# Kernel optimization log

Hardware: AMD Instinct MI355X
Metric: run time of the kernel (lower is better)

The kernel has to match this reference:

```python
import jax, jax.numpy as jnp
import numpy as np

B, T, D = 2, 1024, 1024   # batch, seq, d_model
E, F = 8, 4096            # n_experts, expert hidden (4*d_model)


def setup_inputs() -> dict:
    key = jax.random.key(0)
    k1, k2, k3, k4, k5 = jax.random.split(key, 5)
    x = jax.random.normal(k1, (B, T, D), dtype=jnp.float32)
    token_mask = jax.random.randint(k2, (B, T), 0, 2).astype(jnp.int32)
    router_w = jax.random.normal(k3, (E, D), dtype=jnp.float32) * (1.0 / np.sqrt(D))
    w1 = jax.random.normal(k4, (E, D, F), dtype=jnp.float32) * (1.0 / np.sqrt(D))
    w2 = jax.random.normal(k5, (E, F, D), dtype=jnp.float32) * (1.0 / np.sqrt(F))
    return {"x": x, "token_mask": token_mask, "router_w": router_w, "w1": w1, "w2": w2}


def reference(x, token_mask, router_w, w1, w2):
    b, t, d = x.shape
    n_exp = router_w.shape[0]
    xf = x.reshape(b * t, d)                       # [N, D]
    # top-1 router
    logits = xf @ router_w.T                       # [N, E]
    probs = jax.nn.softmax(logits, axis=-1)
    expert_idx = jnp.argmax(probs, axis=-1)        # [N]
    gate = jnp.take_along_axis(probs, expert_idx[:, None], axis=1)[:, 0]  # [N]
    # expert FFNs: each token routed to exactly one expert (dense masked combine)
    y = jnp.zeros_like(xf)
    for e in range(n_exp):
        he = jnp.maximum(xf @ w1[e], 0.0) @ w2[e]  # [N, D]
        y = jnp.where(expert_idx[:, None] == e, he, y)
    # gate scaling + token masking (masked rows stay exactly zero,
    # matching torch's zero-init y_flat_all + index_copy_)
    mask = token_mask.reshape(b * t).astype(x.dtype)
    out = y * (gate * mask)[:, None]
    return out.reshape(b, t, d)
```

## Files before the change

### kernel.cpp

```cpp
#include <hip/hip_runtime.h>
#include <hip/hip_bf16.h>

#define NTOK 2048
#define DM 1024
#define NEXP 8
#define FFN 4096
#define BM 64
#define BN 64
#define BK 64
#define ASTR 72
#define MT1 8
#define G2_SPLIT 4

typedef __bf16 bf16x8 __attribute__((ext_vector_type(8)));
typedef __bf16 bf16x4 __attribute__((ext_vector_type(4)));
typedef float f32x4 __attribute__((ext_vector_type(4)));

__device__ __forceinline__ bf16x8 zero8() {
  bf16x8 z;
#pragma unroll
  for (int j = 0; j < 8; j++) z[j] = (__bf16)0.f;
  return z;
}

__device__ __forceinline__ bf16x8 readB(const char* BsB, int row, int kh, int quad) {
  return *(const bf16x8*)(BsB + row * 144 +
                          ((((kh << 2) + quad) ^ (row >> 3)) << 4));
}

#define STOREB4() do {                                                   \
    const float* p0 = (const float*)&br0;                                \
    const float* p1 = (const float*)&br1;                                \
    const float* p2 = (const float*)&br2;                                \
    const float* p3 = (const float*)&br3;                                \
    _Pragma("unroll") for (int c = 0; c < 4; ++c) {                      \
      bf16x4 o;                                                          \
      o[0] = (__bf16)p0[c]; o[1] = (__bf16)p1[c];                        \
      o[2] = (__bf16)p2[c]; o[3] = (__bf16)p3[c];                        \
      *(bf16x4*)(bb + c * 144) = o;                                      \
    } } while (0)

__global__ __launch_bounds__(256) void router_gather(
    const float* __restrict__ x, const int* __restrict__ mask,
    const float* __restrict__ rw, int* __restrict__ counts,
    int* __restrict__ tlist, float* __restrict__ gateE,
    __bf16* __restrict__ xg)
{
  int wid = threadIdx.x >> 6, lane = threadIdx.x & 63;
  int t = blockIdx.x * 4 + wid;

  const float* xr = x + (size_t)t * DM;
  float xv[16];
#pragma unroll
  for (int i = 0; i < 4; i++) {
    const float4 v = *(const float4*)(xr + lane * 16 + i * 4);
    xv[i * 4 + 0] = v.x; xv[i * 4 + 1] = v.y;
    xv[i * 4 + 2] = v.z; xv[i * 4 + 3] = v.w;
  }

  float acc[NEXP];
#pragma unroll
  for (int e = 0; e < NEXP; e++) {
    float a = 0.f;
    const float* rwe = rw + e * DM + lane * 16;
#pragma unroll
    for (int i = 0; i < 4; i++) {
      const float4 r = *(const float4*)(rwe + i * 4);
      a += xv[i*4+0]*r.x + xv[i*4+1]*r.y + xv[i*4+2]*r.z + xv[i*4+3]*r.w;
    }
    acc[e] = a;
  }
#pragma unroll
  for (int e = 0; e < NEXP; e++)
#pragma unroll
    for (int s = 1; s < 64; s <<= 1) acc[e] += __shfl_xor(acc[e], s, 64);

  int pack = -1;
  if (lane == 0 && mask[t] != 0) {
    float m = acc[0]; int am = 0;
#pragma unroll
    for (int e = 1; e < NEXP; e++) if (acc[e] > m) { m = acc[e]; am = e; }
    float s = 0.f;
#pragma unroll
    for (int e = 0; e < NEXP; e++) s += __expf(acc[e] - m);
    int slot = atomicAdd(&counts[am], 1);
    tlist[am * NTOK + slot] = t;
    gateE[am * NTOK + slot] = 1.0f / s;
    pack = am * NTOK + slot;
  }
  pack = __shfl(pack, 0, 64);
  if (pack >= 0) {
    __bf16* dst = xg + (size_t)pack * DM + lane * 16;
    bf16x8 o0, o1;
#pragma unroll
    for (int j = 0; j < 8; j++) {
      o0[j] = (__bf16)xv[j];
      o1[j] = (__bf16)xv[8 + j];
    }
    *(bf16x8*)dst = o0;
    *(bf16x8*)(dst + 8) = o1;
  }
}

__global__ __launch_bounds__(256) void moe_gemm1(
    const __bf16* __restrict__ xg, const float* __restrict__ w1,
    const int* __restrict__ counts, const int* __restrict__ tlist,
    __bf16* __restrict__ h)
{
  int bx = blockIdx.x;
  int nt = bx & 63, mt = (bx >> 6) & (MT1 - 1), e = bx >> 9;
  int cnt = counts[e];
  if (mt * BM >= cnt) return;
  int n0 = nt * BN;

  __shared__ __bf16 As[BM][ASTR];
  __shared__ char   Bs[64 * 144];
  __shared__ int    toks[BM];

  int tid = threadIdx.x, lane = tid & 63, w = tid >> 6;
  int wm = w >> 1, wn = w & 1;
  int r16 = lane & 15, quad = lane >> 4;
  int rsw = r16 >> 1;
  char* bb = Bs + (r16 << 2) * 144 +
             (((((w << 1) + (quad >> 1))) ^ rsw) << 4) + ((quad & 1) << 3);

  const __bf16* xge = xg + (size_t)e * NTOK * DM;
  const float*  w1e = w1 + (size_t)e * DM * FFN;

  int ar = tid >> 2;
  int ak = (tid & 3) << 4;
  const float* bptr = w1e + (size_t)(w * 16 + quad * 4) * FFN + n0 + (r16 << 2);

  bf16x8 a0r, a1r;
  float4 br0, br1, br2, br3;

#define LOADG1(kb) do {                                                   \
    a0r = av ? *(const bf16x8*)(aptr + (kb))     : zero8();               \
    a1r = av ? *(const bf16x8*)(aptr + (kb) + 8) : zero8();               \
    br0 = *(const float4*)(bptr + (size_t)((kb) + 0) * FFN);              \
    br1 = *(const float4*)(bptr + (size_t)((kb) + 1) * FFN);              \
    br2 = *(const float4*)(bptr + (size_t)((kb) + 2) * FFN);              \
    br3 = *(const float4*)(bptr + (size_t)((kb) + 3) * FFN);              \
  } while (0)

  for (int m0 = mt * BM; m0 < cnt; m0 += MT1 * BM) {
    bool av = (m0 + ar) < cnt;
    const __bf16* aptr = xge + (size_t)(m0 + ar) * DM + ak;

    f32x4 acc[2][2] = {};
    LOADG1(0);
    const int T = DM / BK;
    for (int t = 0; t < T; t++) {
      *(bf16x8*)&As[ar][ak]     = a0r;
      *(bf16x8*)&As[ar][ak + 8] = a1r;
      STOREB4();
      __syncthreads();
      if (t + 1 < T) LOADG1((t + 1) * BK);
#pragma unroll
      for (int kh = 0; kh < 2; kh++) {
        int ks = kh * 32 + (quad << 3);
        bf16x8 aA = *(const bf16x8*)&As[wm * 32 + r16][ks];
        bf16x8 aB = *(const bf16x8*)&As[wm * 32 + 16 + r16][ks];
        bf16x8 bA = readB(Bs, wn * 32 + r16, kh, quad);
        bf16x8 bB = readB(Bs, wn * 32 + 16 + r16, kh, quad);
        acc[0][0] = __builtin_amdgcn_mfma_f32_16x16x32_bf16(aA, bA, acc[0][0], 0, 0, 0);
        acc[0][1] = __builtin_amdgcn_mfma_f32_16x16x32_bf16(aA, bB, acc[0][1], 0, 0, 0);
        acc[1][0] = __builtin_amdgcn_mfma_f32_16x16x32_bf16(aB, bA, acc[1][0], 0, 0, 0);
        acc[1][1] = __builtin_amdgcn_mfma_f32_16x16x32_bf16(aB, bB, acc[1][1], 0, 0, 0);
      }
      __syncthreads();
    }

    if (tid < BM) toks[tid] = (m0 + tid < cnt) ? tlist[e * NTOK + m0 + tid] : -1;
    __syncthreads();

#pragma unroll
    for (int mf = 0; mf < 2; mf++) {
#pragma unroll
      for (int i = 0; i < 4; i++) {
        int row = wm * 32 + mf * 16 + (quad << 2) + i;
        int tok = toks[row];
        if (tok >= 0) {
          __bf16* hp = h + (size_t)tok * FFN + n0 + wn * 32 + r16;
          hp[0]  = (__bf16)fmaxf(acc[mf][0][i], 0.f);
          hp[16] = (__bf16)fmaxf(acc[mf][1][i], 0.f);
        }
      }
    }
    __syncthreads();
  }
#undef LOADG1
}

__global__ __launch_bounds__(256) void moe_gemm2(
    const __bf16* __restrict__ h, const float* __restrict__ w2,
    const int* __restrict__ counts, const int* __restrict__ tlist,
    const float* __restrict__ gateE, float* __restrict__ out)
{
  int bx = blockIdx.x;
  int nt = bx & 15, mt = (bx >> 4) & (MT1 - 1), e = (bx >> 7) & 7, sp = bx >> 10;
  int cnt = counts[e];
  if (mt * BM >= cnt) return;
  int n0 = nt * BN;
  int ksp = sp * (FFN / G2_SPLIT);

  __shared__ __bf16 As[BM][ASTR];
  __shared__ char   Bs[64 * 144];
  __shared__ int    toks[BM];
  __shared__ float  gts[BM];

  int tid = threadIdx.x, lane = tid & 63, w = tid >> 6;
  int wm = w >> 1, wn = w & 1;
  int r16 = lane & 15, quad = lane >> 4;
  int rsw = r16 >> 1;
  char* bb = Bs + (r16 << 2) * 144 +
             (((((w << 1) + (quad >> 1))) ^ rsw) << 4) + ((quad & 1) << 3);

  const float* w2e = w2 + (size_t)e * FFN * DM;
  int ar = tid >> 2;
  int ak = (tid & 3) << 4;
  const float* bptr = w2e + (size_t)(ksp + w * 16 + quad * 4) * DM + n0 + (r16 << 2);

  bf16x8 a0r, a1r;
  float4 br0, br1, br2, br3;

#define LOADG2(kb) do {                                                   \
    a0r = av ? *(const bf16x8*)(aptr + (kb))     : zero8();               \
    a1r = av ? *(const bf16x8*)(aptr + (kb) + 8) : zero8();               \
    br0 = *(const float4*)(bptr + (size_t)((kb) + 0) * DM);               \
    br1 = *(const float4*)(bptr + (size_t)((kb) + 1) * DM);               \
    br2 = *(const float4*)(bptr + (size_t)((kb) + 2) * DM);               \
    br3 = *(const float4*)(bptr + (size_t)((kb) + 3) * DM);               \
  } while (0)

  for (int m0 = mt * BM; m0 < cnt; m0 += MT1 * BM) {
    if (tid < BM) {
      bool v = (m0 + tid) < cnt;
      toks[tid] = v ? tlist[e * NTOK + m0 + tid] : -1;
      gts[tid]  = v ? gateE[e * NTOK + m0 + tid] : 0.f;
    }
    __syncthreads();

    int tok0 = toks[ar];
    bool av = tok0 >= 0;
    const __bf16* aptr = h + (size_t)(av ? tok0 : 0) * FFN + ksp + ak;

    f32x4 acc[2][2] = {};
    LOADG2(0);
    const int T = (FFN / G2_SPLIT) / BK;
    for (int t = 0; t < T; t++) {
      *(bf16x8*)&As[ar][ak]     = a0r;
      *(bf16x8*)&As[ar][ak + 8] = a1r;
      STOREB4();
      __syncthreads();
      if (t + 1 < T) LOADG2((t + 1) * BK);
#pragma unroll
      for (int kh = 0; kh < 2; kh++) {
        int ks = kh * 32 + (quad << 3);
        bf16x8 aA = *(const bf16x8*)&As[wm * 32 + r16][ks];
        bf16x8 aB = *(const bf16x8*)&As[wm * 32 + 16 + r16][ks];
        bf16x8 bA = readB(Bs, wn * 32 + r16, kh, quad);
        bf16x8 bB = readB(Bs, wn * 32 + 16 + r16, kh, quad);
        acc[0][0] = __builtin_amdgcn_mfma_f32_16x16x32_bf16(aA, bA, acc[0][0], 0, 0, 0);
        acc[0][1] = __builtin_amdgcn_mfma_f32_16x16x32_bf16(aA, bB, acc[0][1], 0, 0, 0);
        acc[1][0] = __builtin_amdgcn_mfma_f32_16x16x32_bf16(aB, bA, acc[1][0], 0, 0, 0);
        acc[1][1] = __builtin_amdgcn_mfma_f32_16x16x32_bf16(aB, bB, acc[1][1], 0, 0, 0);
      }
      __syncthreads();
    }

#pragma unroll
    for (int mf = 0; mf < 2; mf++) {
#pragma unroll
      for (int i = 0; i < 4; i++) {
        int row = wm * 32 + mf * 16 + (quad << 2) + i;
        int tok = toks[row];
        if (tok >= 0) {
          float g = gts[row];
          float* op = out + (size_t)tok * DM + n0 + wn * 32 + r16;
          __hip_atomic_fetch_add(op, acc[mf][0][i] * g,
                                 __ATOMIC_RELAXED, __HIP_MEMORY_SCOPE_AGENT);
          __hip_atomic_fetch_add(op + 16, acc[mf][1][i] * g,
                                 __ATOMIC_RELAXED, __HIP_MEMORY_SCOPE_AGENT);
        }
      }
    }
    __syncthreads();
  }
#undef LOADG2
}

extern "C" void kernel_launch(void* const* d_in, const int* in_sizes, int n_in,
                              void* d_out, int out_size, void* d_ws, size_t ws_size,
                              hipStream_t stream) {
  const float* x    = (const float*)d_in[0];
  const int*   mask = (const int*)d_in[1];
  const float* rw   = (const float*)d_in[2];
  const float* w1   = (const float*)d_in[3];
  const float* w2   = (const float*)d_in[4];
  float* out = (float*)d_out;

  char* ws = (char*)d_ws;
  int*    counts = (int*)ws;
  int*    tlist  = (int*)(ws + 1024);
  float*  gateE  = (float*)(ws + 1024 + 65536);
  __bf16* xg     = (__bf16*)(ws + 132096);
  __bf16* h      = (__bf16*)(ws + 132096 +
                             (size_t)NEXP * NTOK * DM * 2);

  hipMemsetAsync(counts, 0, 1024, stream);
  hipMemsetAsync(out, 0, (size_t)out_size * sizeof(float), stream);

  router_gather<<<NTOK / 4, 256, 0, stream>>>(x, mask, rw, counts, tlist, gateE, xg);
  moe_gemm1<<<NEXP * MT1 * (FFN / BN), 256, 0, stream>>>(xg, w1, counts, tlist, h);
  moe_gemm2<<<G2_SPLIT * NEXP * MT1 * (DM / BN), 256, 0, stream>>>(
      h, w2, counts, tlist, gateE, out);
}
```

Before: 124.6 us.

## Double-buffer LDS tiles and shrink M-tile grid with interleaved block mapping

Both expert GEMMs now keep two LDS buffers for the A and B tiles and prefetch two K-steps ahead, so each iteration needs one barrier instead of two and global loads overlap the MFMA work. The grid drops from 8 M-tile slots per expert/N-tile to 2, each block looping over more token tiles. Block indices are remapped so the two M-slots of neighbouring N-tiles interleave. Launch bounds also request 4 blocks per CU. This cuts blocks that exit immediately but adds LDS use and register pressure, and gives each block more serial work.

```diff
diff --git a/kernel.cpp b/kernel.cpp
--- a/kernel.cpp
+++ b/kernel.cpp
@@ -9,8 +9,8 @@
 #define BN 64
 #define BK 64
 #define ASTR 72
-#define MT1 8
 #define G2_SPLIT 4
+#define BBYTES 9216
 
 typedef __bf16 bf16x8 __attribute__((ext_vector_type(8)));
 typedef __bf16 bf16x4 __attribute__((ext_vector_type(4)));
@@ -28,7 +28,7 @@
                           ((((kh << 2) + quad) ^ (row >> 3)) << 4));
 }
 
-#define STOREB4() do {                                                   \
+#define STOREB4(bbp) do {                                                \
     const float* p0 = (const float*)&br0;                                \
     const float* p1 = (const float*)&br1;                                \
     const float* p2 = (const float*)&br2;                                \
@@ -37,7 +37,7 @@
       bf16x4 o;                                                          \
       o[0] = (__bf16)p0[c]; o[1] = (__bf16)p1[c];                        \
       o[2] = (__bf16)p2[c]; o[3] = (__bf16)p3[c];                        \
-      *(bf16x4*)(bb + c * 144) = o;                                      \
+      *(bf16x4*)((bbp) + c * 144) = o;                                   \
     } } while (0)
 
 __global__ __launch_bounds__(256) void router_gather(
@@ -102,27 +102,29 @@
   }
 }
 
-__global__ __launch_bounds__(256) void moe_gemm1(
+__global__ __launch_bounds__(256, 4) void moe_gemm1(
     const __bf16* __restrict__ xg, const float* __restrict__ w1,
     const int* __restrict__ counts, const int* __restrict__ tlist,
     __bf16* __restrict__ h)
 {
   int bx = blockIdx.x;
-  int nt = bx & 63, mt = (bx >> 6) & (MT1 - 1), e = bx >> 9;
+  int low3 = bx & 7, mt = (bx >> 3) & 1;
+  int idx = ((bx >> 4) << 3) | low3;
+  int e = idx >> 6, nt = idx & 63;
   int cnt = counts[e];
   if (mt * BM >= cnt) return;
   int n0 = nt * BN;
 
-  __shared__ __bf16 As[BM][ASTR];
-  __shared__ char   Bs[64 * 144];
+  __shared__ __bf16 As[2][BM][ASTR];
+  __shared__ char   Bs[2][BBYTES];
   __shared__ int    toks[BM];
 
   int tid = threadIdx.x, lane = tid & 63, w = tid >> 6;
   int wm = w >> 1, wn = w & 1;
   int r16 = lane & 15, quad = lane >> 4;
   int rsw = r16 >> 1;
-  char* bb = Bs + (r16 << 2) * 144 +
-             (((((w << 1) + (quad >> 1))) ^ rsw) << 4) + ((quad & 1) << 3);
+  char* bb0 = Bs[0] + (r16 << 2) * 144 +
+              (((((w << 1) + (quad >> 1))) ^ rsw) << 4) + ((quad & 1) << 3);
 
   const __bf16* xge = xg + (size_t)e * NTOK * DM;
   const float*  w1e = w1 + (size_t)e * DM * FFN;
@@ -143,31 +145,40 @@
     br3 = *(const float4*)(bptr + (size_t)((kb) + 3) * FFN);              \
   } while (0)
 
-  for (int m0 = mt * BM; m0 < cnt; m0 += MT1 * BM) {
+#define WRITEAB1(PAR) do {                                                \
+    *(bf16x8*)&As[PAR][ar][ak]     = a0r;                                 \
+    *(bf16x8*)&As[PAR][ar][ak + 8] = a1r;                                 \
+    STOREB4(bb0 + (PAR) * BBYTES);                                        \
+  } while (0)
+
+#define MFMA8(PAR) do {                                                   \
+    _Pragma("unroll") for (int kh = 0; kh < 2; kh++) {                    \
+      int ks = kh * 32 + (quad << 3);                                     \
+      bf16x8 aA = *(const bf16x8*)&As[PAR][wm * 32 + r16][ks];            \
+      bf16x8 aB = *(const bf16x8*)&As[PAR][wm * 32 + 16 + r16][ks];       \
+      bf16x8 bA = readB(Bs[PAR], wn * 32 + r16, kh, quad);                \
+      bf16x8 bB = readB(Bs[PAR], wn * 32 + 16 + r16, kh, quad);           \
+      acc[0][0] = __builtin_amdgcn_mfma_f32_16x16x32_bf16(aA, bA, acc[0][0], 0, 0, 0); \
+      acc[0][1] = __builtin_amdgcn_mfma_f32_16x16x32_bf16(aA, bB, acc[0][1], 0, 0, 0); \
+      acc[1][0] = __builtin_amdgcn_mfma_f32_16x16x32_bf16(aB, bA, acc[1][0], 0, 0, 0); \
+      acc[1][1] = __builtin_amdgcn_mfma_f32_16x16x32_bf16(aB, bB, acc[1][1], 0, 0, 0); \
+    } } while (0)
+
+  for (int m0 = mt * BM; m0 < cnt; m0 += 2 * BM) {
     bool av = (m0 + ar) < cnt;
     const __bf16* aptr = xge + (size_t)(m0 + ar) * DM + ak;
 
     f32x4 acc[2][2] = {};
     LOADG1(0);
+    WRITEAB1(0);
+    LOADG1(BK);
+    __syncthreads();
     const int T = DM / BK;
     for (int t = 0; t < T; t++) {
-      *(bf16x8*)&As[ar][ak]     = a0r;
-      *(bf16x8*)&As[ar][ak + 8] = a1r;
-      STOREB4();
-      __syncthreads();
-      if (t + 1 < T) LOADG1((t + 1) * BK);
-#pragma unroll
-      for (int kh = 0; kh < 2; kh++) {
-        int ks = kh * 32 + (quad << 3);
-        bf16x8 aA = *(const bf16x8*)&As[wm * 32 + r16][ks];
-        bf16x8 aB = *(const bf16x8*)&As[wm * 32 + 16 + r16][ks];
-        bf16x8 bA = readB(Bs, wn * 32 + r16, kh, quad);
-        bf16x8 bB = readB(Bs, wn * 32 + 16 + r16, kh, quad);
-        acc[0][0] = __builtin_amdgcn_mfma_f32_16x16x32_bf16(aA, bA, acc[0][0], 0, 0, 0);
-        acc[0][1] = __builtin_amdgcn_mfma_f32_16x16x32_bf16(aA, bB, acc[0][1], 0, 0, 0);
-        acc[1][0] = __builtin_amdgcn_mfma_f32_16x16x32_bf16(aB, bA, acc[1][0], 0, 0, 0);
-        acc[1][1] = __builtin_amdgcn_mfma_f32_16x16x32_bf16(aB, bB, acc[1][1], 0, 0, 0);
-      }
+      const int par = t & 1;
+      if (t + 1 < T) WRITEAB1(par ^ 1);
+      if (t + 2 < T) LOADG1((t + 2) * BK);
+      MFMA8(par);
       __syncthreads();
     }
 
@@ -189,23 +200,27 @@
     }
     __syncthreads();
   }
+#undef MFMA8
+#undef WRITEAB1
 #undef LOADG1
 }
 
-__global__ __launch_bounds__(256) void moe_gemm2(
+__global__ __launch_bounds__(256, 4) void moe_gemm2(
     const __bf16* __restrict__ h, const float* __restrict__ w2,
     const int* __restrict__ counts, const int* __restrict__ tlist,
     const float* __restrict__ gateE, float* __restrict__ out)
 {
   int bx = blockIdx.x;
-  int nt = bx & 15, mt = (bx >> 4) & (MT1 - 1), e = (bx >> 7) & 7, sp = bx >> 10;
+  int low3 = bx & 7, mt = (bx >> 3) & 1;
+  int idx = ((bx >> 4) << 3) | low3;
+  int nt = idx & 15, e = (idx >> 4) & 7, sp = idx >> 7;
   int cnt = counts[e];
   if (mt * BM >= cnt) return;
   int n0 = nt * BN;
   int ksp = sp * (FFN / G2_SPLIT);
 
-  __shared__ __bf16 As[BM][ASTR];
-  __shared__ char   Bs[64 * 144];
+  __shared__ __bf16 As[2][BM][ASTR];
+  __shared__ char   Bs[2][BBYTES];
   __shared__ int    toks[BM];
   __shared__ float  gts[BM];
 
@@ -213,8 +228,8 @@
   int wm = w >> 1, wn = w & 1;
   int r16 = lane & 15, quad = lane >> 4;
   int rsw = r16 >> 1;
-  char* bb = Bs + (r16 << 2) * 144 +
-             (((((w << 1) + (quad >> 1))) ^ rsw) << 4) + ((quad & 1) << 3);
+  char* bb0 = Bs[0] + (r16 << 2) * 144 +
+              (((((w << 1) + (quad >> 1))) ^ rsw) << 4) + ((quad & 1) << 3);
 
   const float* w2e = w2 + (size_t)e * FFN * DM;
   int ar = tid >> 2;
@@ -233,7 +248,26 @@
     br3 = *(const float4*)(bptr + (size_t)((kb) + 3) * DM);               \
   } while (0)
 
-  for (int m0 = mt * BM; m0 < cnt; m0 += MT1 * BM) {
+#define WRITEAB2(PAR) do {                                                \
+    *(bf16x8*)&As[PAR][ar][ak]     = a0r;                                 \
+    *(bf16x8*)&As[PAR][ar][ak + 8] = a1r;                                 \
+    STOREB4(bb0 + (PAR) * BBYTES);                                        \
+  } while (0)
+
+#define MFMA8(PAR) do {                                                   \
+    _Pragma("unroll") for (int kh = 0; kh < 2; kh++) {                    \
+      int ks = kh * 32 + (quad << 3);                                     \
+      bf16x8 aA = *(const bf16x8*)&As[PAR][wm * 32 + r16][ks];            \
+      bf16x8 aB = *(const bf16x8*)&As[PAR][wm * 32 + 16 + r16][ks];       \
+      bf16x8 bA = readB(Bs[PAR], wn * 32 + r16, kh, quad);                \
+      bf16x8 bB = readB(Bs[PAR], wn * 32 + 16 + r16, kh, quad);           \
+      acc[0][0] = __builtin_amdgcn_mfma_f32_16x16x32_bf16(aA, bA, acc[0][0], 0, 0, 0); \
+      acc[0][1] = __builtin_amdgcn_mfma_f32_16x16x32_bf16(aA, bB, acc[0][1], 0, 0, 0); \
+      acc[1][0] = __builtin_amdgcn_mfma_f32_16x16x32_bf16(aB, bA, acc[1][0], 0, 0, 0); \
+      acc[1][1] = __builtin_amdgcn_mfma_f32_16x16x32_bf16(aB, bB, acc[1][1], 0, 0, 0); \
+    } } while (0)
+
+  for (int m0 = mt * BM; m0 < cnt; m0 += 2 * BM) {
     if (tid < BM) {
       bool v = (m0 + tid) < cnt;
       toks[tid] = v ? tlist[e * NTOK + m0 + tid] : -1;
@@ -247,25 +281,15 @@
 
     f32x4 acc[2][2] = {};
     LOADG2(0);
+    WRITEAB2(0);
+    LOADG2(BK);
+    __syncthreads();
     const int T = (FFN / G2_SPLIT) / BK;
     for (int t = 0; t < T; t++) {
-      *(bf16x8*)&As[ar][ak]     = a0r;
-      *(bf16x8*)&As[ar][ak + 8] = a1r;
-      STOREB4();
-      __syncthreads();
-      if (t + 1 < T) LOADG2((t + 1) * BK);
-#pragma unroll
-      for (int kh = 0; kh < 2; kh++) {
-        int ks = kh * 32 + (quad << 3);
-        bf16x8 aA = *(const bf16x8*)&As[wm * 32 + r16][ks];
-        bf16x8 aB = *(const bf16x8*)&As[wm * 32 + 16 + r16][ks];
-        bf16x8 bA = readB(Bs, wn * 32 + r16, kh, quad);
-        bf16x8 bB = readB(Bs, wn * 32 + 16 + r16, kh, quad);
-        acc[0][0] = __builtin_amdgcn_mfma_f32_16x16x32_bf16(aA, bA, acc[0][0], 0, 0, 0);
-        acc[0][1] = __builtin_amdgcn_mfma_f32_16x16x32_bf16(aA, bB, acc[0][1], 0, 0, 0);
-        acc[1][0] = __builtin_amdgcn_mfma_f32_16x16x32_bf16(aB, bA, acc[1][0], 0, 0, 0);
-        acc[1][1] = __builtin_amdgcn_mfma_f32_16x16x32_bf16(aB, bB, acc[1][1], 0, 0, 0);
-      }
+      const int par = t & 1;
+      if (t + 1 < T) WRITEAB2(par ^ 1);
+      if (t + 2 < T) LOADG2((t + 2) * BK);
+      MFMA8(par);
       __syncthreads();
     }
 
@@ -287,6 +311,8 @@
     }
     __syncthreads();
   }
+#undef MFMA8
+#undef WRITEAB2
 #undef LOADG2
 }
 
@@ -312,7 +338,6 @@
   hipMemsetAsync(out, 0, (size_t)out_size * sizeof(float), stream);
 
   router_gather<<<NTOK / 4, 256, 0, stream>>>(x, mask, rw, counts, tlist, gateE, xg);
-  moe_gemm1<<<NEXP * MT1 * (FFN / BN), 256, 0, stream>>>(xg, w1, counts, tlist, h);
-  moe_gemm2<<<G2_SPLIT * NEXP * MT1 * (DM / BN), 256, 0, stream>>>(
-      h, w2, counts, tlist, gateE, out);
-}
+  moe_gemm1<<<1024, 256, 0, stream>>>(xg, w1, counts, tlist, h);
+  moe_gemm2<<<1024, 256, 0, stream>>>(h, w2, counts, tlist, gateE, out);
+}
```

Result: slower. 203.6 us (+63.5%).

## Replace split-K atomic accumulation with partial buffers and a separate reduce kernel

Applied to the files above, without the earlier changes.

GEMM2 now stores its four split-K partial results as plain fp32 writes into a workspace buffer instead of issuing relaxed atomic adds into the output. A new reduce4 kernel sums the four partials and applies the per-token gate, which the router writes into a dense, zero-initialised per-token array. The output memset is dropped in favour of zeroing the small gate array. In exchange the change adds a kernel launch and about 64 MB of extra global traffic. Rows for masked tokens are never written to the partial buffer, so the reduce relies on multiplying leftover workspace contents by a zero gate, which produces NaN if that memory holds NaN.

```diff
diff --git a/kernel.cpp b/kernel.cpp
--- a/kernel.cpp
+++ b/kernel.cpp
@@ -44,7 +44,7 @@
     const float* __restrict__ x, const int* __restrict__ mask,
     const float* __restrict__ rw, int* __restrict__ counts,
     int* __restrict__ tlist, float* __restrict__ gateE,
-    __bf16* __restrict__ xg)
+    float* __restrict__ g_dense, __bf16* __restrict__ xg)
 {
   int wid = threadIdx.x >> 6, lane = threadIdx.x & 63;
   int t = blockIdx.x * 4 + wid;
@@ -85,7 +85,9 @@
     for (int e = 0; e < NEXP; e++) s += __expf(acc[e] - m);
     int slot = atomicAdd(&counts[am], 1);
     tlist[am * NTOK + slot] = t;
-    gateE[am * NTOK + slot] = 1.0f / s;
+    float g = 1.0f / s;
+    gateE[am * NTOK + slot] = g;
+    g_dense[t] = g;
     pack = am * NTOK + slot;
   }
   pack = __shfl(pack, 0, 64);
@@ -195,7 +197,7 @@
 __global__ __launch_bounds__(256) void moe_gemm2(
     const __bf16* __restrict__ h, const float* __restrict__ w2,
     const int* __restrict__ counts, const int* __restrict__ tlist,
-    const float* __restrict__ gateE, float* __restrict__ out)
+    float* __restrict__ part)
 {
   int bx = blockIdx.x;
   int nt = bx & 15, mt = (bx >> 4) & (MT1 - 1), e = (bx >> 7) & 7, sp = bx >> 10;
@@ -207,7 +209,6 @@
   __shared__ __bf16 As[BM][ASTR];
   __shared__ char   Bs[64 * 144];
   __shared__ int    toks[BM];
-  __shared__ float  gts[BM];
 
   int tid = threadIdx.x, lane = tid & 63, w = tid >> 6;
   int wm = w >> 1, wn = w & 1;
@@ -220,6 +221,7 @@
   int ar = tid >> 2;
   int ak = (tid & 3) << 4;
   const float* bptr = w2e + (size_t)(ksp + w * 16 + quad * 4) * DM + n0 + (r16 << 2);
+  float* psp = part + (size_t)sp * NTOK * DM;
 
   bf16x8 a0r, a1r;
   float4 br0, br1, br2, br3;
@@ -235,9 +237,7 @@
 
   for (int m0 = mt * BM; m0 < cnt; m0 += MT1 * BM) {
     if (tid < BM) {
-      bool v = (m0 + tid) < cnt;
-      toks[tid] = v ? tlist[e * NTOK + m0 + tid] : -1;
-      gts[tid]  = v ? gateE[e * NTOK + m0 + tid] : 0.f;
+      toks[tid] = (m0 + tid < cnt) ? tlist[e * NTOK + m0 + tid] : -1;
     }
     __syncthreads();
 
@@ -276,18 +276,35 @@
         int row = wm * 32 + mf * 16 + (quad << 2) + i;
         int tok = toks[row];
         if (tok >= 0) {
-          float g = gts[row];
-          float* op = out + (size_t)tok * DM + n0 + wn * 32 + r16;
-          __hip_atomic_fetch_add(op, acc[mf][0][i] * g,
-                                 __ATOMIC_RELAXED, __HIP_MEMORY_SCOPE_AGENT);
-          __hip_atomic_fetch_add(op + 16, acc[mf][1][i] * g,
-                                 __ATOMIC_RELAXED, __HIP_MEMORY_SCOPE_AGENT);
+          float* pp = psp + (size_t)tok * DM + n0 + wn * 32 + r16;
+          pp[0]  = acc[mf][0][i];
+          pp[16] = acc[mf][1][i];
         }
       }
     }
     __syncthreads();
   }
 #undef LOADG2
+}
+
+__global__ __launch_bounds__(256) void reduce4(
+    const float* __restrict__ part, const float* __restrict__ gd,
+    float* __restrict__ out)
+{
+  int i = blockIdx.x * 256 + threadIdx.x;
+  const size_t SPSTRIDE = (size_t)NTOK * DM / 4;
+  const float4* p = (const float4*)part;
+  float4 a = p[i];
+  float4 b = p[i + SPSTRIDE];
+  float4 c = p[i + 2 * SPSTRIDE];
+  float4 d = p[i + 3 * SPSTRIDE];
+  float g = gd[i >> 8];
+  float4 r;
+  r.x = g * (a.x + b.x + c.x + d.x);
+  r.y = g * (a.y + b.y + c.y + d.y);
+  r.z = g * (a.z + b.z + c.z + d.z);
+  r.w = g * (a.w + b.w + c.w + d.w);
+  ((float4*)out)[i] = r;
 }
 
 extern "C" void kernel_launch(void* const* d_in, const int* in_sizes, int n_in,
@@ -301,18 +318,24 @@
   float* out = (float*)d_out;
 
   char* ws = (char*)d_ws;
-  int*    counts = (int*)ws;
-  int*    tlist  = (int*)(ws + 1024);
-  float*  gateE  = (float*)(ws + 1024 + 65536);
-  __bf16* xg     = (__bf16*)(ws + 132096);
-  __bf16* h      = (__bf16*)(ws + 132096 +
-                             (size_t)NEXP * NTOK * DM * 2);
+  int*    counts  = (int*)ws;
+  int*    tlist   = (int*)(ws + 1024);
+  float*  gateE   = (float*)(ws + 1024 + 65536);
+  float*  g_dense = (float*)(ws + 1024 + 131072);
+  __bf16* xg      = (__bf16*)(ws + 140544);
+  __bf16* h       = (__bf16*)(ws + 140544 +
+                              (size_t)NEXP * NTOK * DM * 2);
+  float*  part    = (float*)(ws + 140544 +
+                             (size_t)NEXP * NTOK * DM * 2 +
+                             (size_t)NTOK * FFN * 2);
 
   hipMemsetAsync(counts, 0, 1024, stream);
-  hipMemsetAsync(out, 0, (size_t)out_size * sizeof(float), stream);
-
-  router_gather<<<NTOK / 4, 256, 0, stream>>>(x, mask, rw, counts, tlist, gateE, xg);
+  hipMemsetAsync(g_dense, 0, NTOK * sizeof(float), stream);
+
+  router_gather<<<NTOK / 4, 256, 0, stream>>>(x, mask, rw, counts, tlist, gateE,
+                                              g_dense, xg);
   moe_gemm1<<<NEXP * MT1 * (FFN / BN), 256, 0, stream>>>(xg, w1, counts, tlist, h);
   moe_gemm2<<<G2_SPLIT * NEXP * MT1 * (DM / BN), 256, 0, stream>>>(
-      h, w2, counts, tlist, gateE, out);
-}
+      h, w2, counts, tlist, part);
+  reduce4<<<NTOK * DM / 4 / 256, 256, 0, stream>>>(part, g_dense, out);
+}
```

Result: slower. 134.1 us (+7.6%).

## Store expert hidden activations compactly per expert and interleave experts across blocks

Applied to the files above, without the earlier changes.

Adds a tiny scan kernel that computes per-expert offsets. GEMM1 then writes hidden activations contiguously in expert-sorted order instead of scattering them by token index, and GEMM2 reads those rows directly without a token indirection. The block index decoding now puts the expert in the low bits, so consecutive blocks spread across experts and the early-exit work imbalance is more even. The cost is an extra single-thread kernel launch on the critical path.

```diff
diff --git a/kernel.cpp b/kernel.cpp
--- a/kernel.cpp
+++ b/kernel.cpp
@@ -102,20 +102,28 @@
   }
 }
 
+__global__ void scan_offs(const int* __restrict__ counts, int* __restrict__ offs) {
+  if (threadIdx.x == 0) {
+    int s = 0;
+#pragma unroll
+    for (int e = 0; e < NEXP; e++) { offs[e] = s; s += counts[e]; }
+  }
+}
+
 __global__ __launch_bounds__(256) void moe_gemm1(
     const __bf16* __restrict__ xg, const float* __restrict__ w1,
-    const int* __restrict__ counts, const int* __restrict__ tlist,
-    __bf16* __restrict__ h)
+    const int* __restrict__ counts, const int* __restrict__ offs,
+    __bf16* __restrict__ hc)
 {
   int bx = blockIdx.x;
-  int nt = bx & 63, mt = (bx >> 6) & (MT1 - 1), e = bx >> 9;
+  int e = bx & 7, nt = (bx >> 3) & 63, mt = bx >> 9;
   int cnt = counts[e];
   if (mt * BM >= cnt) return;
   int n0 = nt * BN;
+  int hbase = offs[e];
 
   __shared__ __bf16 As[BM][ASTR];
   __shared__ char   Bs[64 * 144];
-  __shared__ int    toks[BM];
 
   int tid = threadIdx.x, lane = tid & 63, w = tid >> 6;
   int wm = w >> 1, wn = w & 1;
@@ -171,17 +179,13 @@
       __syncthreads();
     }
 
-    if (tid < BM) toks[tid] = (m0 + tid < cnt) ? tlist[e * NTOK + m0 + tid] : -1;
-    __syncthreads();
-
 #pragma unroll
     for (int mf = 0; mf < 2; mf++) {
 #pragma unroll
       for (int i = 0; i < 4; i++) {
         int row = wm * 32 + mf * 16 + (quad << 2) + i;
-        int tok = toks[row];
-        if (tok >= 0) {
-          __bf16* hp = h + (size_t)tok * FFN + n0 + wn * 32 + r16;
+        if (m0 + row < cnt) {
+          __bf16* hp = hc + (size_t)(hbase + m0 + row) * FFN + n0 + wn * 32 + r16;
           hp[0]  = (__bf16)fmaxf(acc[mf][0][i], 0.f);
           hp[16] = (__bf16)fmaxf(acc[mf][1][i], 0.f);
         }
@@ -193,16 +197,18 @@
 }
 
 __global__ __launch_bounds__(256) void moe_gemm2(
-    const __bf16* __restrict__ h, const float* __restrict__ w2,
-    const int* __restrict__ counts, const int* __restrict__ tlist,
-    const float* __restrict__ gateE, float* __restrict__ out)
+    const __bf16* __restrict__ hc, const float* __restrict__ w2,
+    const int* __restrict__ counts, const int* __restrict__ offs,
+    const int* __restrict__ tlist, const float* __restrict__ gateE,
+    float* __restrict__ out)
 {
   int bx = blockIdx.x;
-  int nt = bx & 15, mt = (bx >> 4) & (MT1 - 1), e = (bx >> 7) & 7, sp = bx >> 10;
+  int e = bx & 7, nt = (bx >> 3) & 15, mt = (bx >> 7) & 7, sp = bx >> 10;
   int cnt = counts[e];
   if (mt * BM >= cnt) return;
   int n0 = nt * BN;
   int ksp = sp * (FFN / G2_SPLIT);
+  int hbase = offs[e];
 
   __shared__ __bf16 As[BM][ASTR];
   __shared__ char   Bs[64 * 144];
@@ -241,9 +247,8 @@
     }
     __syncthreads();
 
-    int tok0 = toks[ar];
-    bool av = tok0 >= 0;
-    const __bf16* aptr = h + (size_t)(av ? tok0 : 0) * FFN + ksp + ak;
+    bool av = (m0 + ar) < cnt;
+    const __bf16* aptr = hc + (size_t)(hbase + (av ? m0 + ar : 0)) * FFN + ksp + ak;
 
     f32x4 acc[2][2] = {};
     LOADG2(0);
@@ -302,17 +307,19 @@
 
   char* ws = (char*)d_ws;
   int*    counts = (int*)ws;
-  int*    tlist  = (int*)(ws + 1024);
-  float*  gateE  = (float*)(ws + 1024 + 65536);
-  __bf16* xg     = (__bf16*)(ws + 132096);
-  __bf16* h      = (__bf16*)(ws + 132096 +
+  int*    offs   = (int*)(ws + 1024);
+  int*    tlist  = (int*)(ws + 2048);
+  float*  gateE  = (float*)(ws + 2048 + 65536);
+  __bf16* xg     = (__bf16*)(ws + 139264);
+  __bf16* hc     = (__bf16*)(ws + 139264 +
                              (size_t)NEXP * NTOK * DM * 2);
 
   hipMemsetAsync(counts, 0, 1024, stream);
   hipMemsetAsync(out, 0, (size_t)out_size * sizeof(float), stream);
 
   router_gather<<<NTOK / 4, 256, 0, stream>>>(x, mask, rw, counts, tlist, gateE, xg);
-  moe_gemm1<<<NEXP * MT1 * (FFN / BN), 256, 0, stream>>>(xg, w1, counts, tlist, h);
+  scan_offs<<<1, 64, 0, stream>>>(counts, offs);
+  moe_gemm1<<<NEXP * MT1 * (FFN / BN), 256, 0, stream>>>(xg, w1, counts, offs, hc);
   moe_gemm2<<<G2_SPLIT * NEXP * MT1 * (DM / BN), 256, 0, stream>>>(
-      h, w2, counts, tlist, gateE, out);
-}
+      hc, w2, counts, offs, tlist, gateE, out);
+}
```

After: 129.2 us. +3.7%, slower.
